# Optimization experiments

Hardware: AMD Instinct MI355X
Metric: run time of the kernel (lower is better)

## Reference

```python
import jax, jax.numpy as jnp
import numpy as np

# --- static config (matches init_kwargs / input_specs) ---
N_GRAPHS = 32
NODES = 1000          # num_nodes per graph
N = N_GRAPHS * NODES  # 32000 total nodes
F_IN = 128            # num_features
E_DIM = 16            # edge_attr_dim
H, C = 4, 16          # heads, GAT_dim
HC = H * C            # 64
E = 512000            # edges (before self-loops)
PROJ = 8              # proj_nodes
OUT = 256             # output_dim
NEG_SLOPE = 0.2       # PyG GATConv default


def setup_inputs() -> dict:
    key = jax.random.key(0)
    ks = jax.random.split(key, 20)
    s = 0.1
    return {
        "x": jax.random.normal(ks[0], (N, F_IN), jnp.float32),
        "edge_attr": jax.random.normal(ks[1], (E, E_DIM), jnp.float32),
        # layer 0 (input_conv): F_IN -> H*C
        "W0":   jax.random.normal(ks[2], (F_IN, HC), jnp.float32) * s,
        "a_s0": jax.random.normal(ks[3], (H, C), jnp.float32) * s,
        "a_d0": jax.random.normal(ks[4], (H, C), jnp.float32) * s,
        "W_e0": jax.random.normal(ks[5], (E_DIM, HC), jnp.float32) * s,
        "a_e0": jax.random.normal(ks[6], (H, C), jnp.float32) * s,
        "b0":   jnp.zeros((HC,), jnp.float32),
        # layers 1..2 stacked: HC -> H*C
        "Wg":   jax.random.normal(ks[7], (2, HC, HC), jnp.float32) * s,
        "a_sg": jax.random.normal(ks[8], (2, H, C), jnp.float32) * s,
        "a_dg": jax.random.normal(ks[9], (2, H, C), jnp.float32) * s,
        "W_eg": jax.random.normal(ks[10], (2, E_DIM, HC), jnp.float32) * s,
        "a_eg": jax.random.normal(ks[11], (2, H, C), jnp.float32) * s,
        "bg":   jnp.zeros((2, HC), jnp.float32),
        # node_proj: HC -> PROJ ; fc_out: NODES*PROJ -> OUT
        "Wp": jax.random.normal(ks[12], (HC, PROJ), jnp.float32) * s,
        "bp": jnp.zeros((PROJ,), jnp.float32),
        "Wo": jax.random.normal(ks[13], (NODES * PROJ, OUT), jnp.float32) * (s / 4),
        "bo": jnp.zeros((OUT,), jnp.float32),
        "edge_index": jax.random.randint(ks[14], (2, E), 0, N, jnp.int32),
        "batch": jnp.repeat(jnp.arange(N_GRAPHS, dtype=jnp.int32), NODES),
    }


def _gat_layer(x, src, dst, eattr, W, a_s, a_d, W_e, a_e, b):
    """PyG GATConv (concat=True, shared src/dst lin, edge_dim) forward."""
    xl = (x @ W).reshape(N, H, C)                       # [N,H,C]
    al_s = jnp.sum(xl * a_s, axis=-1)                   # [N,H]
    al_d = jnp.sum(xl * a_d, axis=-1)                   # [N,H]
    el = (eattr @ W_e).reshape(-1, H, C)                # [Ef,H,C]
    al_e = jnp.sum(el * a_e, axis=-1)                   # [Ef,H]
    logits = jax.nn.leaky_relu(al_s[src] + al_d[dst] + al_e, NEG_SLOPE)
    # segment softmax over destination nodes (every node has a self-loop)
    mx = jax.ops.segment_max(logits, dst, num_segments=N)
    p = jnp.exp(logits - mx[dst])
    denom = jax.ops.segment_sum(p, dst, num_segments=N)
    alpha = p / denom[dst]                               # [Ef,H]
    out = jax.ops.segment_sum(xl[src] * alpha[..., None], dst, num_segments=N)
    return out.reshape(N, HC) + b


def reference(x, edge_attr, W0, a_s0, a_d0, W_e0, a_e0, b0,
              Wg, a_sg, a_dg, W_eg, a_eg, bg,
              Wp, bp, Wo, bo, edge_index, batch):
    src, dst = edge_index[0], edge_index[1]
    # PyG add_self_loops with fill_value='mean': per-dst mean of incoming edge_attr
    deg = jax.ops.segment_sum(jnp.ones((E,), edge_attr.dtype), dst, num_segments=N)
    loop_attr = jax.ops.segment_sum(edge_attr, dst, num_segments=N) / jnp.maximum(deg, 1.0)[:, None]
    loops = jnp.arange(N, dtype=src.dtype)
    src_f = jnp.concatenate([src, loops])
    dst_f = jnp.concatenate([dst, loops])
    ea_f = jnp.concatenate([edge_attr, loop_attr], axis=0)   # [E+N, E_DIM]

    h = jax.nn.relu(_gat_layer(x, src_f, dst_f, ea_f, W0, a_s0, a_d0, W_e0, a_e0, b0))
    for i in range(2):
        h = jax.nn.relu(_gat_layer(h, src_f, dst_f, ea_f,
                                   Wg[i], a_sg[i], a_dg[i], W_eg[i], a_eg[i], bg[i]))
    h = jax.nn.relu(h @ Wp + bp)                             # [N, PROJ]
    B = batch.shape[0] // NODES                              # static batch count
    h = h.reshape(B, NODES * PROJ)
    return h @ Wo + bo                                       # [B, OUT]
```

## Files before the change

kernel.cpp:

```cpp
#include <hip/hip_runtime.h>
#include <hip/hip_bf16.h>

#define N_NODES 32000
#define FIN     128
#define E_EDGES 512000
#define EF_EDGES 544000
#define HC      64
#define NGRAPH  32
#define PROJ    8
#define OUT_DIM 256

static __device__ inline unsigned short f2bf(float f) {
  unsigned int x = __float_as_uint(f);
  unsigned int r = (x + 0x7fffu + ((x >> 16) & 1u)) >> 16;
  return (unsigned short)r;
}
static __device__ inline float bf2f(unsigned short u) {
  return __uint_as_float((unsigned int)u << 16);
}

__global__ __launch_bounds__(256) void zero_kernel(int* __restrict__ deg) {
  deg[blockIdx.x * 256 + threadIdx.x] = 0;
}

__global__ __launch_bounds__(256) void deg_kernel(const int* __restrict__ ei,
                                                  int* __restrict__ deg) {
  int e = blockIdx.x * 256 + threadIdx.x;
  atomicAdd(&deg[ei[E_EDGES + e]], 1);
}

__global__ __launch_bounds__(256) void scan1_kernel(const int* __restrict__ deg,
                                                    int* __restrict__ offs,
                                                    int* __restrict__ bsum) {
  int idx = blockIdx.x * 256 + threadIdx.x;
  int lane = threadIdx.x & 63;
  int w = threadIdx.x >> 6;
  int v = deg[idx] + 1;
  int s = v;
#pragma unroll
  for (int off = 1; off < 64; off <<= 1) {
    int t = __shfl_up(s, off);
    if (lane >= off) s += t;
  }
  __shared__ int wsum[4];
  if (lane == 63) wsum[w] = s;
  __syncthreads();
  int add = 0;
#pragma unroll
  for (int i = 0; i < 4; ++i) add += (i < w) ? wsum[i] : 0;
  int incl = s + add;
  offs[idx] = incl - v;
  if (threadIdx.x == 255) bsum[blockIdx.x] = incl;
}

__global__ __launch_bounds__(128) void scan2_kernel(const int* __restrict__ bsum,
                                                    int* __restrict__ boffs,
                                                    int* __restrict__ offs) {
  int t = threadIdx.x;
  int lane = t & 63;
  int w = t >> 6;
  int v = (t < 125) ? bsum[t] : 0;
  int s = v;
#pragma unroll
  for (int off = 1; off < 64; off <<= 1) {
    int tt = __shfl_up(s, off);
    if (lane >= off) s += tt;
  }
  __shared__ int wsum[2];
  if (lane == 63) wsum[w] = s;
  __syncthreads();
  int incl = s + ((w == 1) ? wsum[0] : 0);
  if (t < 125) boffs[t] = incl - v;
  if (t == 127) offs[N_NODES] = incl;
}

__global__ __launch_bounds__(256) void scan3_kernel(const int* __restrict__ boffs,
                                                    int* __restrict__ offs,
                                                    int* __restrict__ nxt) {
  int idx = blockIdx.x * 256 + threadIdx.x;
  int o = offs[idx] + boffs[blockIdx.x];
  offs[idx] = o;
  nxt[idx] = o;
}

__global__ __launch_bounds__(256) void fill_kernel(const int* __restrict__ ei,
                                                   int* __restrict__ nxt,
                                                   int* __restrict__ csr_src,
                                                   int* __restrict__ csr_eid,
                                                   int* __restrict__ csr_pos) {
  int e = blockIdx.x * 256 + threadIdx.x;
  int s, d;
  if (e < E_EDGES) { s = ei[e]; d = ei[E_EDGES + e]; }
  else             { s = e - E_EDGES; d = s; }
  int pos = atomicAdd(&nxt[d], 1);
  csr_src[pos] = s;
  csr_eid[pos] = e;
  csr_pos[e] = pos;
}

__global__ __launch_bounds__(256) void loopattr_kernel(const int* __restrict__ offs,
                                                       const int* __restrict__ csr_eid,
                                                       const float* __restrict__ ea,
                                                       float* __restrict__ loop_attr) {
  int lane = threadIdx.x & 63;
  int n = blockIdx.x * 4 + (threadIdx.x >> 6);
  int k = lane & 15, g = lane >> 4;
  int beg = offs[n], end = offs[n + 1];
  float s = 0.f;
  for (int i = beg + g; i < end; i += 4) {
    int e = csr_eid[i];
    if (e < E_EDGES) s += ea[(size_t)e * 16 + k];
  }
  s += __shfl_xor(s, 16);
  s += __shfl_xor(s, 32);
  int degv = end - beg - 1;
  if (g == 0) loop_attr[(size_t)n * 16 + k] = s / fmaxf((float)degv, 1.f);
}

template <int K>
__global__ __launch_bounds__(256) void transform_kernel(const float* __restrict__ A,
                                                        const float* __restrict__ W,
                                                        const float* __restrict__ a_s,
                                                        const float* __restrict__ a_d,
                                                        unsigned short* __restrict__ xlb,
                                                        float* __restrict__ al_s,
                                                        float* __restrict__ al_d) {
  __shared__ float sW[64][64];
  __shared__ float sA[64][65];
  int tid = threadIdx.x;
  int row0 = blockIdx.x * 64;
  int tx = tid & 15, ty = tid >> 4;
  int c0 = tx * 4, r0 = ty * 4;
  float acc[4][4] = {};
  for (int kc = 0; kc < K; kc += 64) {
    for (int i = tid; i < 1024; i += 256) {
      int kk = i >> 4, c4 = (i & 15) * 4;
      *(float4*)&sW[kk][c4] = *(const float4*)&W[(size_t)(kc + kk) * HC + c4];
    }
    for (int i = tid; i < 1024; i += 256) {
      int r = i >> 4, k4 = (i & 15) * 4;
      float4 v = *(const float4*)&A[(size_t)(row0 + r) * K + kc + k4];
      sA[r][k4 + 0] = v.x; sA[r][k4 + 1] = v.y;
      sA[r][k4 + 2] = v.z; sA[r][k4 + 3] = v.w;
    }
    __syncthreads();
#pragma unroll 8
    for (int kk = 0; kk < 64; ++kk) {
      float4 w = *(float4*)&sW[kk][c0];
      float a0 = sA[r0 + 0][kk];
      float a1 = sA[r0 + 1][kk];
      float a2 = sA[r0 + 2][kk];
      float a3 = sA[r0 + 3][kk];
      acc[0][0] = fmaf(a0, w.x, acc[0][0]); acc[0][1] = fmaf(a0, w.y, acc[0][1]);
      acc[0][2] = fmaf(a0, w.z, acc[0][2]); acc[0][3] = fmaf(a0, w.w, acc[0][3]);
      acc[1][0] = fmaf(a1, w.x, acc[1][0]); acc[1][1] = fmaf(a1, w.y, acc[1][1]);
      acc[1][2] = fmaf(a1, w.z, acc[1][2]); acc[1][3] = fmaf(a1, w.w, acc[1][3]);
      acc[2][0] = fmaf(a2, w.x, acc[2][0]); acc[2][1] = fmaf(a2, w.y, acc[2][1]);
      acc[2][2] = fmaf(a2, w.z, acc[2][2]); acc[2][3] = fmaf(a2, w.w, acc[2][3]);
      acc[3][0] = fmaf(a3, w.x, acc[3][0]); acc[3][1] = fmaf(a3, w.y, acc[3][1]);
      acc[3][2] = fmaf(a3, w.z, acc[3][2]); acc[3][3] = fmaf(a3, w.w, acc[3][3]);
    }
    __syncthreads();
  }
  float asv[4], adv[4];
#pragma unroll
  for (int j = 0; j < 4; ++j) { asv[j] = a_s[c0 + j]; adv[j] = a_d[c0 + j]; }
  int hd = tx >> 2;
#pragma unroll
  for (int i = 0; i < 4; ++i) {
    int r = row0 + r0 + i;
    ushort4 u = make_ushort4(f2bf(acc[i][0]), f2bf(acc[i][1]),
                             f2bf(acc[i][2]), f2bf(acc[i][3]));
    *(ushort4*)&xlb[(size_t)r * HC + c0] = u;
    float ps = acc[i][0] * asv[0] + acc[i][1] * asv[1] + acc[i][2] * asv[2] + acc[i][3] * asv[3];
    float pd = acc[i][0] * adv[0] + acc[i][1] * adv[1] + acc[i][2] * adv[2] + acc[i][3] * adv[3];
    ps += __shfl_xor(ps, 1); ps += __shfl_xor(ps, 2);
    pd += __shfl_xor(pd, 1); pd += __shfl_xor(pd, 2);
    if ((tx & 3) == 0) {
      al_s[(size_t)r * 4 + hd] = ps;
      al_d[(size_t)r * 4 + hd] = pd;
    }
  }
}

__global__ __launch_bounds__(256) void logit_kernel(const float* __restrict__ edge_attr,
                                                    const float* __restrict__ loop_attr,
                                                    const float* __restrict__ W_e,
                                                    const float* __restrict__ a_e,
                                                    const int* __restrict__ ei,
                                                    const int* __restrict__ csr_pos,
                                                    const float* __restrict__ al_s,
                                                    float* __restrict__ lg0) {
  __shared__ float sMe[16][4];
  int tid = threadIdx.x;
  if (tid < 64) {
    int d = tid >> 2, h = tid & 3;
    float s = 0.f;
#pragma unroll
    for (int c = 0; c < 16; ++c) s += W_e[d * HC + h * 16 + c] * a_e[h * 16 + c];
    sMe[d][h] = s;
  }
  __syncthreads();
  int e = blockIdx.x * 256 + tid;
  int src;
  const float* ea;
  if (e < E_EDGES) { src = ei[e];          ea = &edge_attr[(size_t)e * 16]; }
  else             { src = e - E_EDGES;    ea = &loop_attr[(size_t)(e - E_EDGES) * 16]; }
  float4 v0 = *(const float4*)(ea + 0);
  float4 v1 = *(const float4*)(ea + 4);
  float4 v2 = *(const float4*)(ea + 8);
  float4 v3 = *(const float4*)(ea + 12);
  float4 als = *(const float4*)&al_s[(size_t)src * 4];
  float r[4];
#pragma unroll
  for (int h = 0; h < 4; ++h) {
    r[h] = v0.x * sMe[0][h] + v0.y * sMe[1][h] + v0.z * sMe[2][h] + v0.w * sMe[3][h] +
           v1.x * sMe[4][h] + v1.y * sMe[5][h] + v1.z * sMe[6][h] + v1.w * sMe[7][h] +
           v2.x * sMe[8][h] + v2.y * sMe[9][h] + v2.z * sMe[10][h] + v2.w * sMe[11][h] +
           v3.x * sMe[12][h] + v3.y * sMe[13][h] + v3.z * sMe[14][h] + v3.w * sMe[15][h];
  }
  int pos = csr_pos[e];
  *(float4*)&lg0[(size_t)pos * 4] =
      make_float4(r[0] + als.x, r[1] + als.y, r[2] + als.z, r[3] + als.w);
}

template <int FUSE_PROJ>
__global__ __launch_bounds__(256) void gather_kernel(const int* __restrict__ offs,
                                                     const int* __restrict__ csr_src,
                                                     const float* __restrict__ lg0,
                                                     const unsigned short* __restrict__ xlb,
                                                     const float* __restrict__ al_d,
                                                     const float* __restrict__ bias,
                                                     const float* __restrict__ Wp,
                                                     const float* __restrict__ bp,
                                                     float* __restrict__ outp) {
  int lane = threadIdx.x & 63;
  int n = blockIdx.x * 4 + (threadIdx.x >> 6);
  int hd = lane >> 4;
  int beg = offs[n], end = offs[n + 1];
  float ald = al_d[(size_t)n * 4 + hd];
  float m = -1e30f, denom = 0.f, acc = 0.f;
  int i = beg;
  for (; i + 4 <= end; i += 4) {
    int s0 = csr_src[i + 0];
    int s1 = csr_src[i + 1];
    int s2 = csr_src[i + 2];
    int s3 = csr_src[i + 3];
    float l0 = lg0[(size_t)(i + 0) * 4 + hd] + ald;
    float l1 = lg0[(size_t)(i + 1) * 4 + hd] + ald;
    float l2 = lg0[(size_t)(i + 2) * 4 + hd] + ald;
    float l3 = lg0[(size_t)(i + 3) * 4 + hd] + ald;
    l0 = (l0 > 0.f) ? l0 : 0.2f * l0;
    l1 = (l1 > 0.f) ? l1 : 0.2f * l1;
    l2 = (l2 > 0.f) ? l2 : 0.2f * l2;
    l3 = (l3 > 0.f) ? l3 : 0.2f * l3;
    unsigned short x0 = xlb[(size_t)s0 * HC + lane];
    unsigned short x1 = xlb[(size_t)s1 * HC + lane];
    unsigned short x2 = xlb[(size_t)s2 * HC + lane];
    unsigned short x3 = xlb[(size_t)s3 * HC + lane];
    float mx = fmaxf(fmaxf(fmaxf(l0, l1), fmaxf(l2, l3)), m);
    float sc = __expf(m - mx);
    float p0 = __expf(l0 - mx);
    float p1 = __expf(l1 - mx);
    float p2 = __expf(l2 - mx);
    float p3 = __expf(l3 - mx);
    denom = denom * sc + ((p0 + p1) + (p2 + p3));
    acc = acc * sc + p0 * bf2f(x0) + p1 * bf2f(x1) + p2 * bf2f(x2) + p3 * bf2f(x3);
    m = mx;
  }
  for (; i < end; ++i) {
    int s = csr_src[i];
    float l = lg0[(size_t)i * 4 + hd] + ald;
    l = (l > 0.f) ? l : 0.2f * l;
    float mx = fmaxf(m, l);
    float sc = __expf(m - mx);
    float p = __expf(l - mx);
    denom = denom * sc + p;
    acc = acc * sc + p * bf2f(xlb[(size_t)s * HC + lane]);
    m = mx;
  }
  float hv = fmaxf(acc / denom + bias[lane], 0.f);
  if constexpr (!FUSE_PROJ) {
    outp[(size_t)n * HC + lane] = hv;
  } else {
    float pj[8];
#pragma unroll
    for (int j = 0; j < 8; ++j) pj[j] = hv * Wp[lane * PROJ + j];
#pragma unroll
    for (int off = 1; off < 64; off <<= 1) {
#pragma unroll
      for (int j = 0; j < 8; ++j) pj[j] += __shfl_xor(pj[j], off);
    }
    if (lane < 8) {
      float v = pj[0];
      v = (lane == 1) ? pj[1] : v;
      v = (lane == 2) ? pj[2] : v;
      v = (lane == 3) ? pj[3] : v;
      v = (lane == 4) ? pj[4] : v;
      v = (lane == 5) ? pj[5] : v;
      v = (lane == 6) ? pj[6] : v;
      v = (lane == 7) ? pj[7] : v;
      outp[(size_t)n * PROJ + lane] = fmaxf(v + bp[lane], 0.f);
    }
  }
}

__global__ __launch_bounds__(256) void fc1_kernel(const float* __restrict__ p,
                                                  const float* __restrict__ Wo,
                                                  float* __restrict__ part) {
  __shared__ float sp[NGRAPH][250];
  int kc = blockIdx.x;
  int ct = blockIdx.y;
  int tid = threadIdx.x;
  for (int i = tid; i < NGRAPH * 250; i += 256) {
    int g = i / 250, kk = i % 250;
    sp[g][kk] = p[(size_t)g * 8000 + kc * 250 + kk];
  }
  __syncthreads();
  int c = ct * 64 + (tid & 63);
  int kg = tid >> 6;
  float acc[NGRAPH] = {};
  for (int kk = kg; kk < 250; kk += 4) {
    float w = Wo[(size_t)(kc * 250 + kk) * OUT_DIM + c];
#pragma unroll
    for (int g = 0; g < NGRAPH; ++g) acc[g] = fmaf(sp[g][kk], w, acc[g]);
  }
  int ch = kc * 4 + kg;
#pragma unroll
  for (int g = 0; g < NGRAPH; ++g)
    part[((size_t)ch * NGRAPH + g) * OUT_DIM + c] = acc[g];
}

__global__ __launch_bounds__(256) void fc2_kernel(const float* __restrict__ part,
                                                  const float* __restrict__ bo,
                                                  float* __restrict__ out) {
  int i = blockIdx.x * 256 + threadIdx.x;
  int g = i >> 8, c = i & 255;
  float s = bo[c];
  for (int ch = 0; ch < 128; ++ch) s += part[((size_t)ch * NGRAPH + g) * OUT_DIM + c];
  out[i] = s;
}

extern "C" void kernel_launch(void* const* d_in, const int* in_sizes, int n_in,
                              void* d_out, int out_size, void* d_ws, size_t ws_size,
                              hipStream_t stream) {
  const float* x         = (const float*)d_in[0];
  const float* edge_attr = (const float*)d_in[1];
  const float* W0        = (const float*)d_in[2];
  const float* a_s0      = (const float*)d_in[3];
  const float* a_d0      = (const float*)d_in[4];
  const float* W_e0      = (const float*)d_in[5];
  const float* a_e0      = (const float*)d_in[6];
  const float* b0        = (const float*)d_in[7];
  const float* Wg        = (const float*)d_in[8];
  const float* a_sg      = (const float*)d_in[9];
  const float* a_dg      = (const float*)d_in[10];
  const float* W_eg      = (const float*)d_in[11];
  const float* a_eg      = (const float*)d_in[12];
  const float* bg        = (const float*)d_in[13];
  const float* Wp        = (const float*)d_in[14];
  const float* bp        = (const float*)d_in[15];
  const float* Wo        = (const float*)d_in[16];
  const float* bo        = (const float*)d_in[17];
  const int*   ei        = (const int*)d_in[18];

  char* base = (char*)d_ws;
  size_t off = 0;
  auto alloc = [&](size_t bytes) -> void* {
    void* ptr = base + off;
    off = (off + bytes + 255) & ~(size_t)255;
    return ptr;
  };
  int*            deg       = (int*)alloc((size_t)N_NODES * 4);
  int*            offs      = (int*)alloc((size_t)(N_NODES + 1) * 4);
  int*            nxt       = (int*)alloc((size_t)N_NODES * 4);
  int*            bsum      = (int*)alloc(128 * 4);
  int*            boffs     = (int*)alloc(128 * 4);
  int*            csr_src   = (int*)alloc((size_t)EF_EDGES * 4);
  int*            csr_eid   = (int*)alloc((size_t)EF_EDGES * 4);
  int*            csr_pos   = (int*)alloc((size_t)EF_EDGES * 4);
  float*          loop_attr = (float*)alloc((size_t)N_NODES * 16 * 4);
  float*          lg0       = (float*)alloc((size_t)EF_EDGES * 4 * 4);
  unsigned short* xlb       = (unsigned short*)alloc((size_t)N_NODES * HC * 2);
  float*          al_s      = (float*)alloc((size_t)N_NODES * 4 * 4);
  float*          al_d      = (float*)alloc((size_t)N_NODES * 4 * 4);
  float*          hA        = (float*)alloc((size_t)N_NODES * HC * 4);
  float*          hB        = (float*)alloc((size_t)N_NODES * HC * 4);
  float*          pbuf      = (float*)alloc((size_t)N_NODES * PROJ * 4);
  float*          part      = (float*)alloc((size_t)128 * NGRAPH * OUT_DIM * 4);

  zero_kernel<<<N_NODES / 256, 256, 0, stream>>>(deg);
  deg_kernel<<<E_EDGES / 256, 256, 0, stream>>>(ei, deg);
  scan1_kernel<<<N_NODES / 256, 256, 0, stream>>>(deg, offs, bsum);
  scan2_kernel<<<1, 128, 0, stream>>>(bsum, boffs, offs);
  scan3_kernel<<<N_NODES / 256, 256, 0, stream>>>(boffs, offs, nxt);
  fill_kernel<<<EF_EDGES / 256, 256, 0, stream>>>(ei, nxt, csr_src, csr_eid, csr_pos);
  loopattr_kernel<<<N_NODES / 4, 256, 0, stream>>>(offs, csr_eid, edge_attr, loop_attr);

  transform_kernel<FIN><<<N_NODES / 64, 256, 0, stream>>>(x, W0, a_s0, a_d0, xlb, al_s, al_d);
  logit_kernel<<<EF_EDGES / 256, 256, 0, stream>>>(edge_attr, loop_attr, W_e0, a_e0, ei, csr_pos, al_s, lg0);
  gather_kernel<0><<<N_NODES / 4, 256, 0, stream>>>(offs, csr_src, lg0, xlb, al_d, b0, Wp, bp, hA);

  transform_kernel<HC><<<N_NODES / 64, 256, 0, stream>>>(hA, Wg, a_sg, a_dg, xlb, al_s, al_d);
  logit_kernel<<<EF_EDGES / 256, 256, 0, stream>>>(edge_attr, loop_attr, W_eg, a_eg, ei, csr_pos, al_s, lg0);
  gather_kernel<0><<<N_NODES / 4, 256, 0, stream>>>(offs, csr_src, lg0, xlb, al_d, bg, Wp, bp, hB);

  transform_kernel<HC><<<N_NODES / 64, 256, 0, stream>>>(hB, Wg + HC * HC, a_sg + 64, a_dg + 64, xlb, al_s, al_d);
  logit_kernel<<<EF_EDGES / 256, 256, 0, stream>>>(edge_attr, loop_attr, W_eg + 16 * HC, a_eg + 64, ei, csr_pos, al_s, lg0);
  gather_kernel<1><<<N_NODES / 4, 256, 0, stream>>>(offs, csr_src, lg0, xlb, al_d, bg + 64, Wp, bp, pbuf);

  fc1_kernel<<<dim3(32, 4), 256, 0, stream>>>(pbuf, Wo, part);
  fc2_kernel<<<NGRAPH, 256, 0, stream>>>(part, bo, (float*)d_out);
}
```

Measured before the change: 277.9 us.

## Precompute edge logits for all layers once in fp16 and gather al_s in aggregation

The three per-layer logit kernels are replaced by one kernel that reads each edge's attributes once and writes the edge-attention term for all three layers, stored as fp16 in CSR order. The source-node term al_s is now gathered inside the aggregation kernel instead of being folded into the logit buffer. The change also merges the two-kernel block-offset scan into scan3, which sums the preceding block totals per block, and adds nontemporal loads and stores. This removes two edge-sized passes and halves logit traffic, at the cost of fp16 rounding on the logits and an extra random al_s read per edge in the gather.

```diff
diff --git a/kernel.cpp b/kernel.cpp
--- a/kernel.cpp
+++ b/kernel.cpp
@@ -1,5 +1,6 @@
 #include <hip/hip_runtime.h>
 #include <hip/hip_bf16.h>
+#include <hip/hip_fp16.h>
 
 #define N_NODES 32000
 #define FIN     128
@@ -18,6 +19,12 @@
 static __device__ inline float bf2f(unsigned short u) {
   return __uint_as_float((unsigned int)u << 16);
 }
+static __device__ inline unsigned short f2h(float f) {
+  return __half_as_ushort(__float2half(f));
+}
+static __device__ inline float h2f(unsigned short u) {
+  return __half2float(__ushort_as_half(u));
+}
 
 __global__ __launch_bounds__(256) void zero_kernel(int* __restrict__ deg) {
   deg[blockIdx.x * 256 + threadIdx.x] = 0;
@@ -53,34 +60,23 @@
   if (threadIdx.x == 255) bsum[blockIdx.x] = incl;
 }
 
-__global__ __launch_bounds__(128) void scan2_kernel(const int* __restrict__ bsum,
-                                                    int* __restrict__ boffs,
-                                                    int* __restrict__ offs) {
-  int t = threadIdx.x;
-  int lane = t & 63;
-  int w = t >> 6;
-  int v = (t < 125) ? bsum[t] : 0;
-  int s = v;
-#pragma unroll
-  for (int off = 1; off < 64; off <<= 1) {
-    int tt = __shfl_up(s, off);
-    if (lane >= off) s += tt;
-  }
-  __shared__ int wsum[2];
-  if (lane == 63) wsum[w] = s;
-  __syncthreads();
-  int incl = s + ((w == 1) ? wsum[0] : 0);
-  if (t < 125) boffs[t] = incl - v;
-  if (t == 127) offs[N_NODES] = incl;
-}
-
-__global__ __launch_bounds__(256) void scan3_kernel(const int* __restrict__ boffs,
+__global__ __launch_bounds__(256) void scan3_kernel(const int* __restrict__ bsum,
                                                     int* __restrict__ offs,
                                                     int* __restrict__ nxt) {
-  int idx = blockIdx.x * 256 + threadIdx.x;
-  int o = offs[idx] + boffs[blockIdx.x];
+  __shared__ int wsum[4];
+  int tid = threadIdx.x, bid = blockIdx.x;
+  int lane = tid & 63, w = tid >> 6;
+  int v = (tid < bid) ? bsum[tid] : 0;
+#pragma unroll
+  for (int off = 1; off < 64; off <<= 1) v += __shfl_xor(v, off);
+  if (lane == 0) wsum[w] = v;
+  __syncthreads();
+  int boff = wsum[0] + wsum[1] + wsum[2] + wsum[3];
+  int idx = bid * 256 + tid;
+  int o = offs[idx] + boff;
   offs[idx] = o;
   nxt[idx] = o;
+  if (bid == 0 && tid == 0) offs[N_NODES] = EF_EDGES;
 }
 
 __global__ __launch_bounds__(256) void fill_kernel(const int* __restrict__ ei,
@@ -115,6 +111,56 @@
   s += __shfl_xor(s, 32);
   int degv = end - beg - 1;
   if (g == 0) loop_attr[(size_t)n * 16 + k] = s / fmaxf((float)degv, 1.f);
+}
+
+__global__ __launch_bounds__(256) void elogit_kernel(const float* __restrict__ edge_attr,
+                                                     const float* __restrict__ loop_attr,
+                                                     const float* __restrict__ W_e0,
+                                                     const float* __restrict__ a_e0,
+                                                     const float* __restrict__ W_eg,
+                                                     const float* __restrict__ a_eg,
+                                                     const int* __restrict__ csr_pos,
+                                                     unsigned short* __restrict__ lgE) {
+  __shared__ float sMe[3][16][4];
+  int tid = threadIdx.x;
+  if (tid < 192) {
+    int l = tid >> 6, r6 = tid & 63, d = r6 >> 2, h = r6 & 3;
+    const float* We = (l == 0) ? W_e0 : W_eg + (size_t)(l - 1) * 16 * HC;
+    const float* ae = (l == 0) ? a_e0 : a_eg + (size_t)(l - 1) * 64;
+    float s = 0.f;
+#pragma unroll
+    for (int c = 0; c < 16; ++c) s += We[d * HC + h * 16 + c] * ae[h * 16 + c];
+    sMe[l][d][h] = s;
+  }
+  __syncthreads();
+  int e = blockIdx.x * 256 + tid;
+  const float* ea = (e < E_EDGES) ? &edge_attr[(size_t)e * 16]
+                                  : &loop_attr[(size_t)(e - E_EDGES) * 16];
+  float av[16];
+  *(float4*)&av[0]  = *(const float4*)(ea + 0);
+  *(float4*)&av[4]  = *(const float4*)(ea + 4);
+  *(float4*)&av[8]  = *(const float4*)(ea + 8);
+  *(float4*)&av[12] = *(const float4*)(ea + 12);
+  int pos = csr_pos[e];
+#pragma unroll
+  for (int l = 0; l < 3; ++l) {
+    float r0 = 0.f, r1 = 0.f, r2 = 0.f, r3 = 0.f;
+#pragma unroll
+    for (int d = 0; d < 16; ++d) {
+      float a = av[d];
+      r0 = fmaf(a, sMe[l][d][0], r0);
+      r1 = fmaf(a, sMe[l][d][1], r1);
+      r2 = fmaf(a, sMe[l][d][2], r2);
+      r3 = fmaf(a, sMe[l][d][3], r3);
+    }
+    unsigned long long u =
+        (unsigned long long)f2h(r0) |
+        ((unsigned long long)f2h(r1) << 16) |
+        ((unsigned long long)f2h(r2) << 32) |
+        ((unsigned long long)f2h(r3) << 48);
+    __builtin_nontemporal_store(
+        u, (unsigned long long*)&lgE[((size_t)l * EF_EDGES + pos) * 4]);
+  }
 }
 
 template <int K>
@@ -183,52 +229,12 @@
   }
 }
 
-__global__ __launch_bounds__(256) void logit_kernel(const float* __restrict__ edge_attr,
-                                                    const float* __restrict__ loop_attr,
-                                                    const float* __restrict__ W_e,
-                                                    const float* __restrict__ a_e,
-                                                    const int* __restrict__ ei,
-                                                    const int* __restrict__ csr_pos,
-                                                    const float* __restrict__ al_s,
-                                                    float* __restrict__ lg0) {
-  __shared__ float sMe[16][4];
-  int tid = threadIdx.x;
-  if (tid < 64) {
-    int d = tid >> 2, h = tid & 3;
-    float s = 0.f;
-#pragma unroll
-    for (int c = 0; c < 16; ++c) s += W_e[d * HC + h * 16 + c] * a_e[h * 16 + c];
-    sMe[d][h] = s;
-  }
-  __syncthreads();
-  int e = blockIdx.x * 256 + tid;
-  int src;
-  const float* ea;
-  if (e < E_EDGES) { src = ei[e];          ea = &edge_attr[(size_t)e * 16]; }
-  else             { src = e - E_EDGES;    ea = &loop_attr[(size_t)(e - E_EDGES) * 16]; }
-  float4 v0 = *(const float4*)(ea + 0);
-  float4 v1 = *(const float4*)(ea + 4);
-  float4 v2 = *(const float4*)(ea + 8);
-  float4 v3 = *(const float4*)(ea + 12);
-  float4 als = *(const float4*)&al_s[(size_t)src * 4];
-  float r[4];
-#pragma unroll
-  for (int h = 0; h < 4; ++h) {
-    r[h] = v0.x * sMe[0][h] + v0.y * sMe[1][h] + v0.z * sMe[2][h] + v0.w * sMe[3][h] +
-           v1.x * sMe[4][h] + v1.y * sMe[5][h] + v1.z * sMe[6][h] + v1.w * sMe[7][h] +
-           v2.x * sMe[8][h] + v2.y * sMe[9][h] + v2.z * sMe[10][h] + v2.w * sMe[11][h] +
-           v3.x * sMe[12][h] + v3.y * sMe[13][h] + v3.z * sMe[14][h] + v3.w * sMe[15][h];
-  }
-  int pos = csr_pos[e];
-  *(float4*)&lg0[(size_t)pos * 4] =
-      make_float4(r[0] + als.x, r[1] + als.y, r[2] + als.z, r[3] + als.w);
-}
-
 template <int FUSE_PROJ>
 __global__ __launch_bounds__(256) void gather_kernel(const int* __restrict__ offs,
                                                      const int* __restrict__ csr_src,
-                                                     const float* __restrict__ lg0,
+                                                     const unsigned short* __restrict__ lg,
                                                      const unsigned short* __restrict__ xlb,
+                                                     const float* __restrict__ al_s,
                                                      const float* __restrict__ al_d,
                                                      const float* __restrict__ bias,
                                                      const float* __restrict__ Wp,
@@ -242,14 +248,18 @@
   float m = -1e30f, denom = 0.f, acc = 0.f;
   int i = beg;
   for (; i + 4 <= end; i += 4) {
-    int s0 = csr_src[i + 0];
-    int s1 = csr_src[i + 1];
-    int s2 = csr_src[i + 2];
-    int s3 = csr_src[i + 3];
-    float l0 = lg0[(size_t)(i + 0) * 4 + hd] + ald;
-    float l1 = lg0[(size_t)(i + 1) * 4 + hd] + ald;
-    float l2 = lg0[(size_t)(i + 2) * 4 + hd] + ald;
-    float l3 = lg0[(size_t)(i + 3) * 4 + hd] + ald;
+    int s0 = __builtin_nontemporal_load(&csr_src[i + 0]);
+    int s1 = __builtin_nontemporal_load(&csr_src[i + 1]);
+    int s2 = __builtin_nontemporal_load(&csr_src[i + 2]);
+    int s3 = __builtin_nontemporal_load(&csr_src[i + 3]);
+    unsigned short g0 = __builtin_nontemporal_load(&lg[(size_t)(i + 0) * 4 + hd]);
+    unsigned short g1 = __builtin_nontemporal_load(&lg[(size_t)(i + 1) * 4 + hd]);
+    unsigned short g2 = __builtin_nontemporal_load(&lg[(size_t)(i + 2) * 4 + hd]);
+    unsigned short g3 = __builtin_nontemporal_load(&lg[(size_t)(i + 3) * 4 + hd]);
+    float l0 = h2f(g0) + al_s[(size_t)s0 * 4 + hd] + ald;
+    float l1 = h2f(g1) + al_s[(size_t)s1 * 4 + hd] + ald;
+    float l2 = h2f(g2) + al_s[(size_t)s2 * 4 + hd] + ald;
+    float l3 = h2f(g3) + al_s[(size_t)s3 * 4 + hd] + ald;
     l0 = (l0 > 0.f) ? l0 : 0.2f * l0;
     l1 = (l1 > 0.f) ? l1 : 0.2f * l1;
     l2 = (l2 > 0.f) ? l2 : 0.2f * l2;
@@ -269,14 +279,15 @@
     m = mx;
   }
   for (; i < end; ++i) {
-    int s = csr_src[i];
-    float l = lg0[(size_t)i * 4 + hd] + ald;
+    int s = __builtin_nontemporal_load(&csr_src[i]);
+    unsigned short g = __builtin_nontemporal_load(&lg[(size_t)i * 4 + hd]);
+    float l = h2f(g) + al_s[(size_t)s * 4 + hd] + ald;
     l = (l > 0.f) ? l : 0.2f * l;
     float mx = fmaxf(m, l);
     float sc = __expf(m - mx);
-    float p = __expf(l - mx);
-    denom = denom * sc + p;
-    acc = acc * sc + p * bf2f(xlb[(size_t)s * HC + lane]);
+    float pp = __expf(l - mx);
+    denom = denom * sc + pp;
+    acc = acc * sc + pp * bf2f(xlb[(size_t)s * HC + lane]);
     m = mx;
   }
   float hv = fmaxf(acc / denom + bias[lane], 0.f);
@@ -321,7 +332,7 @@
   int kg = tid >> 6;
   float acc[NGRAPH] = {};
   for (int kk = kg; kk < 250; kk += 4) {
-    float w = Wo[(size_t)(kc * 250 + kk) * OUT_DIM + c];
+    float w = __builtin_nontemporal_load(&Wo[(size_t)(kc * 250 + kk) * OUT_DIM + c]);
 #pragma unroll
     for (int g = 0; g < NGRAPH; ++g) acc[g] = fmaf(sp[g][kk], w, acc[g]);
   }
@@ -375,12 +386,11 @@
   int*            offs      = (int*)alloc((size_t)(N_NODES + 1) * 4);
   int*            nxt       = (int*)alloc((size_t)N_NODES * 4);
   int*            bsum      = (int*)alloc(128 * 4);
-  int*            boffs     = (int*)alloc(128 * 4);
   int*            csr_src   = (int*)alloc((size_t)EF_EDGES * 4);
   int*            csr_eid   = (int*)alloc((size_t)EF_EDGES * 4);
   int*            csr_pos   = (int*)alloc((size_t)EF_EDGES * 4);
   float*          loop_attr = (float*)alloc((size_t)N_NODES * 16 * 4);
-  float*          lg0       = (float*)alloc((size_t)EF_EDGES * 4 * 4);
+  unsigned short* lgE       = (unsigned short*)alloc((size_t)3 * EF_EDGES * 4 * 2);
   unsigned short* xlb       = (unsigned short*)alloc((size_t)N_NODES * HC * 2);
   float*          al_s      = (float*)alloc((size_t)N_NODES * 4 * 4);
   float*          al_d      = (float*)alloc((size_t)N_NODES * 4 * 4);
@@ -392,22 +402,24 @@
   zero_kernel<<<N_NODES / 256, 256, 0, stream>>>(deg);
   deg_kernel<<<E_EDGES / 256, 256, 0, stream>>>(ei, deg);
   scan1_kernel<<<N_NODES / 256, 256, 0, stream>>>(deg, offs, bsum);
-  scan2_kernel<<<1, 128, 0, stream>>>(bsum, boffs, offs);
-  scan3_kernel<<<N_NODES / 256, 256, 0, stream>>>(boffs, offs, nxt);
+  scan3_kernel<<<N_NODES / 256, 256, 0, stream>>>(bsum, offs, nxt);
   fill_kernel<<<EF_EDGES / 256, 256, 0, stream>>>(ei, nxt, csr_src, csr_eid, csr_pos);
   loopattr_kernel<<<N_NODES / 4, 256, 0, stream>>>(offs, csr_eid, edge_attr, loop_attr);
+  elogit_kernel<<<EF_EDGES / 256, 256, 0, stream>>>(edge_attr, loop_attr, W_e0, a_e0,
+                                                    W_eg, a_eg, csr_pos, lgE);
 
   transform_kernel<FIN><<<N_NODES / 64, 256, 0, stream>>>(x, W0, a_s0, a_d0, xlb, al_s, al_d);
-  logit_kernel<<<EF_EDGES / 256, 256, 0, stream>>>(edge_attr, loop_attr, W_e0, a_e0, ei, csr_pos, al_s, lg0);
-  gather_kernel<0><<<N_NODES / 4, 256, 0, stream>>>(offs, csr_src, lg0, xlb, al_d, b0, Wp, bp, hA);
+  gather_kernel<0><<<N_NODES / 4, 256, 0, stream>>>(offs, csr_src, lgE, xlb,
+                                                    al_s, al_d, b0, Wp, bp, hA);
 
   transform_kernel<HC><<<N_NODES / 64, 256, 0, stream>>>(hA, Wg, a_sg, a_dg, xlb, al_s, al_d);
-  logit_kernel<<<EF_EDGES / 256, 256, 0, stream>>>(edge_attr, loop_attr, W_eg, a_eg, ei, csr_pos, al_s, lg0);
-  gather_kernel<0><<<N_NODES / 4, 256, 0, stream>>>(offs, csr_src, lg0, xlb, al_d, bg, Wp, bp, hB);
-
-  transform_kernel<HC><<<N_NODES / 64, 256, 0, stream>>>(hB, Wg + HC * HC, a_sg + 64, a_dg + 64, xlb, al_s, al_d);
-  logit_kernel<<<EF_EDGES / 256, 256, 0, stream>>>(edge_attr, loop_attr, W_eg + 16 * HC, a_eg + 64, ei, csr_pos, al_s, lg0);
-  gather_kernel<1><<<N_NODES / 4, 256, 0, stream>>>(offs, csr_src, lg0, xlb, al_d, bg + 64, Wp, bp, pbuf);
+  gather_kernel<0><<<N_NODES / 4, 256, 0, stream>>>(offs, csr_src, lgE + (size_t)EF_EDGES * 4,
+                                                    xlb, al_s, al_d, bg, Wp, bp, hB);
+
+  transform_kernel<HC><<<N_NODES / 64, 256, 0, stream>>>(hB, Wg + HC * HC, a_sg + 64,
+                                                         a_dg + 64, xlb, al_s, al_d);
+  gather_kernel<1><<<N_NODES / 4, 256, 0, stream>>>(offs, csr_src, lgE + (size_t)2 * EF_EDGES * 4,
+                                                    xlb, al_s, al_d, bg + 64, Wp, bp, pbuf);
 
   fc1_kernel<<<dim3(32, 4), 256, 0, stream>>>(pbuf, Wo, part);
   fc2_kernel<<<NGRAPH, 256, 0, stream>>>(part, bo, (float*)d_out);
```

Result: slower. 320.3 us (+15.2%).
